# Kernel tuning notes

Hardware: AMD Instinct MI355X
Metric: run time of the kernel (lower is better)

Reference implementation:

```python
import math
import jax, jax.numpy as jnp
import numpy as np

B, S, D = 8, 920, 1536
H, HD = 4, 384            # num heads, head dim; all_head = H*HD = 1536
MAX_POS = 920
L = 2 * MAX_POS - 1       # 1839 relative positions


def setup_inputs() -> dict:
    key = jax.random.key(0)
    k1, k2, k3, k4, k5 = jax.random.split(key, 5)
    return {
        "hidden_states": jax.random.normal(k1, (B, S, D), dtype=jnp.float32),
        "w_query": jax.random.normal(k2, (D, H * HD), dtype=jnp.float32) * 0.02,
        "w_key": jax.random.normal(k3, (D, H * HD), dtype=jnp.float32) * 0.02,
        "w_value": jax.random.normal(k4, (D, H * HD), dtype=jnp.float32) * 0.02,
        "distance_embedding": jax.random.normal(k5, (L, HD), dtype=jnp.float32) * 0.02,
    }


def reshape_fortran(x, shape):
    # Matches torch reference: reverse-permute, C reshape of reversed shape, reverse-permute back.
    x = jnp.transpose(x, tuple(reversed(range(x.ndim))))
    x = jnp.reshape(x, tuple(reversed(shape)))
    return jnp.transpose(x, tuple(reversed(range(len(shape)))))


def relative_position_embedding_rotate(scores):
    # scores: [B, H, L, S]
    scores = jnp.transpose(scores, (0, 2, 3, 1))  # [B, L, S, H]
    b, hs, s, h = scores.shape
    scores = jnp.concatenate([scores, jnp.zeros((b, s, s, h), scores.dtype)], axis=1)
    scores = reshape_fortran(scores, [b, (hs + s) * s, 1, h])
    scores = scores[:, : (s + hs - 1) * s]
    scores = reshape_fortran(scores, [b, hs + s - 1, s, h])
    halfpoint = hs // 2
    scores = scores[:, halfpoint : halfpoint + s]          # [B, S, S, H]
    scores = jnp.transpose(scores, (0, 2, 1, 3))           # transpose(1,2)
    return jnp.transpose(scores, (0, 3, 1, 2))             # [B, H, S, S]


def reference(hidden_states, w_query, w_key, w_value, distance_embedding):
    inv = 1.0 / math.sqrt(HD)
    q = (hidden_states @ w_query) * inv                    # [B, S, H*HD]
    k = hidden_states @ w_key
    v = hidden_states @ w_value

    def heads(x):  # [B,S,H*HD] -> [B,H,S,HD]
        return jnp.transpose(x.reshape(B, S, H, HD), (0, 2, 1, 3))

    q, k, v = heads(q), heads(k), heads(v)

    scores = jnp.einsum("bhqd,bhkd->bhqk", q, k)           # [B,H,S,S]
    rel = jnp.einsum("ld,bhsd->bhls", distance_embedding, q)  # [B,H,L,S]
    scores = scores + relative_position_embedding_rotate(rel)

    probs = jax.nn.softmax(scores, axis=-1)
    ctx = jnp.einsum("bhqk,bhkd->bhqd", probs, v)          # [B,H,S,HD]
    ctx = jnp.transpose(ctx, (0, 2, 1, 3)).reshape(B, S, H * HD)
    return ctx
```

## Files before the change

kernel.cpp:

```cpp
#include <hip/hip_runtime.h>

#define S_LEN 920
#define DMODEL 1536
#define NH 4
#define HD 384
#define LREL 1839
#define BATCH 8
#define MTOT (BATCH * S_LEN)
#define KPAD 960
#define PRLD 1840
#define NBH (BATCH * NH)

#define CHS   5652480UL
#define BSLAB 2826240UL
#define KOFF  1413120UL

#define TP_BH   1692800UL
#define SCPR_BH 3385600UL
#define CHBH    (TP_BH + SCPR_BH)
#define QKV_SCRATCH 36765696UL
#define EB_BYTES 1412352UL
#define VT_BYTES 23592960UL

typedef __attribute__((ext_vector_type(8))) short  s16x8;
typedef __attribute__((ext_vector_type(4))) short  s16x4;
typedef __attribute__((ext_vector_type(8))) __bf16 bf16x8;
typedef __attribute__((ext_vector_type(4))) float  f32x4;

__device__ __forceinline__ short f2b(float x) {
  unsigned u = __builtin_bit_cast(unsigned, x);
  unsigned r = (u + 0x7FFFu + ((u >> 16) & 1u)) >> 16;
  return (short)r;
}
__device__ __forceinline__ float b2f(short s) {
  unsigned u = ((unsigned)(unsigned short)s) << 16;
  return __builtin_bit_cast(float, u);
}

__device__ __forceinline__ void load_lds16(const short* g, short* lds) {
  __builtin_amdgcn_global_load_lds(
      (const __attribute__((address_space(1))) void*)g,
      (__attribute__((address_space(3))) void*)lds, 16, 0, 0);
}

__device__ __forceinline__ f32x4 mfma_bf16(s16x8 a, s16x8 b, f32x4 c) {
  return __builtin_amdgcn_mfma_f32_16x16x32_bf16(
      __builtin_bit_cast(bf16x8, a), __builtin_bit_cast(bf16x8, b), c, 0, 0, 0);
}

__device__ __forceinline__ void gemm_core(short* As, short* Bs,
                                          const short* __restrict__ A, int ldA, int mClamp,
                                          const short* __restrict__ B, int ldB, int nClamp,
                                          int K, int m0, int n0, f32x4 acc[4][4]) {
  const int tid  = threadIdx.x;
  const int w    = tid >> 6;
  const int lane = tid & 63;
  const int lrow = lane >> 3;
  const int lcol = (lane & 7) * 8;
  const int lr   = lane & 15;
  const int lq   = lane >> 4;
  const int wm   = (w >> 1) * 64;
  const int wn   = (w & 1) * 64;

  const short* pa[4];
  const short* pb[4];
  short* la[4];
  short* lb[4];
#pragma unroll
  for (int i = 0; i < 4; ++i) {
    int row = w * 32 + i * 8 + lrow;
    int ra = m0 + row; if (ra > mClamp) ra = mClamp;
    int rb = n0 + row; if (rb > nClamp) rb = nClamp;
    pa[i] = A + (size_t)ra * ldA + lcol;
    pb[i] = B + (size_t)rb * ldB + lcol;
    la[i] = &As[(w * 32 + i * 8) * 64];
    lb[i] = &Bs[(w * 32 + i * 8) * 64];
  }

#pragma unroll
  for (int i = 0; i < 4; ++i)
#pragma unroll
    for (int j = 0; j < 4; ++j) acc[i][j] = (f32x4){0.f, 0.f, 0.f, 0.f};

  for (int k0 = 0; k0 < K; k0 += 64) {
#pragma unroll
    for (int i = 0; i < 4; ++i) {
      load_lds16(pa[i] + k0, la[i]);
      load_lds16(pb[i] + k0, lb[i]);
    }
    __syncthreads();
#pragma unroll
    for (int kk = 0; kk < 2; ++kk) {
      s16x8 af[4], bf[4];
#pragma unroll
      for (int f = 0; f < 4; ++f)
        af[f] = *(const s16x8*)&As[(wm + f * 16 + lr) * 64 + kk * 32 + lq * 8];
#pragma unroll
      for (int f = 0; f < 4; ++f)
        bf[f] = *(const s16x8*)&Bs[(wn + f * 16 + lr) * 64 + kk * 32 + lq * 8];
#pragma unroll
      for (int i = 0; i < 4; ++i)
#pragma unroll
        for (int j = 0; j < 4; ++j)
          acc[i][j] = mfma_bf16(af[i], bf[j], acc[i][j]);
    }
    __syncthreads();
  }
}

__device__ __forceinline__ void gemm_core256(short* As, short* Bs,
                                             const short* __restrict__ A, int ldA, int mClamp,
                                             const short* __restrict__ B, int ldB, int nClamp,
                                             int K, int m0, int n0, f32x4 acc[4][8]) {
  const int tid  = threadIdx.x;
  const int w    = tid >> 6;
  const int lane = tid & 63;
  const int lrow = lane >> 3;
  const int lcol = (lane & 7) * 8;
  const int lr   = lane & 15;
  const int lq   = lane >> 4;
  const int wm   = (w >> 1) * 64;
  const int wn   = (w & 1) * 128;

  const short* pa[4];
  short* la[4];
  const short* pb[8];
  short* lb[8];
#pragma unroll
  for (int i = 0; i < 4; ++i) {
    int row = w * 32 + i * 8 + lrow;
    int ra = m0 + row; if (ra > mClamp) ra = mClamp;
    pa[i] = A + (size_t)ra * ldA + lcol;
    la[i] = &As[(w * 32 + i * 8) * 64];
  }
#pragma unroll
  for (int i = 0; i < 8; ++i) {
    int row = w * 64 + i * 8 + lrow;
    int rb = n0 + row; if (rb > nClamp) rb = nClamp;
    pb[i] = B + (size_t)rb * ldB + lcol;
    lb[i] = &Bs[(w * 64 + i * 8) * 64];
  }

#pragma unroll
  for (int i = 0; i < 4; ++i)
#pragma unroll
    for (int j = 0; j < 8; ++j) acc[i][j] = (f32x4){0.f, 0.f, 0.f, 0.f};

  for (int k0 = 0; k0 < K; k0 += 64) {
#pragma unroll
    for (int i = 0; i < 4; ++i) load_lds16(pa[i] + k0, la[i]);
#pragma unroll
    for (int i = 0; i < 8; ++i) load_lds16(pb[i] + k0, lb[i]);
    __syncthreads();
#pragma unroll
    for (int kk = 0; kk < 2; ++kk) {
      s16x8 af[4], bf[8];
#pragma unroll
      for (int f = 0; f < 4; ++f)
        af[f] = *(const s16x8*)&As[(wm + f * 16 + lr) * 64 + kk * 32 + lq * 8];
#pragma unroll
      for (int f = 0; f < 8; ++f)
        bf[f] = *(const s16x8*)&Bs[(wn + f * 16 + lr) * 64 + kk * 32 + lq * 8];
#pragma unroll
      for (int i = 0; i < 4; ++i)
#pragma unroll
        for (int j = 0; j < 8; ++j)
          acc[i][j] = mfma_bf16(af[i], bf[j], acc[i][j]);
    }
    __syncthreads();
  }
}

__global__ void k_cast(const float* __restrict__ X, short* __restrict__ O, int n4) {
  int i = blockIdx.x * blockDim.x + threadIdx.x;
  if (i >= n4) return;
  float4 v = ((const float4*)X)[i];
  s16x4 o = {f2b(v.x), f2b(v.y), f2b(v.z), f2b(v.w)};
  *(s16x4*)&O[(size_t)i * 4] = o;
}

__global__ void k_transpose_w(const float* __restrict__ W0, const float* __restrict__ W1,
                              const float* __restrict__ W2, short* __restrict__ Wt) {
  const float* W = (blockIdx.z == 0) ? W0 : ((blockIdx.z == 1) ? W1 : W2);
  short* O = Wt + (size_t)blockIdx.z * DMODEL * DMODEL;
  __shared__ float t[32][33];
  int tx = threadIdx.x, ty = threadIdx.y;
  int n0 = blockIdx.x * 32, k0 = blockIdx.y * 32;
#pragma unroll
  for (int i = 0; i < 4; ++i)
    t[ty + i * 8][tx] = W[(size_t)(k0 + ty + i * 8) * DMODEL + n0 + tx];
  __syncthreads();
#pragma unroll
  for (int i = 0; i < 4; ++i)
    O[(size_t)(n0 + ty + i * 8) * DMODEL + k0 + tx] = f2b(t[tx][ty + i * 8]);
}

__global__ void k_zero_vtpad(short* __restrict__ Vt) {
  int idx = blockIdx.x * blockDim.x + threadIdx.x;
  if (idx >= NBH * HD * (KPAD - S_LEN)) return;
  int bhd = idx / (KPAD - S_LEN);
  int s = S_LEN + idx - bhd * (KPAD - S_LEN);
  Vt[(size_t)bhd * KPAD + s] = 0;
}

#define QKV_NT (DMODEL / 64)

__device__ __forceinline__ s16x8 qkv_frag(const short* base, int row, int kk, int lq) {
  int byte = (row << 7) + (kk << 6) + (lq << 4);
  byte ^= (row & 7) << 4;
  return *(const s16x8*)((const char*)base + byte);
}

__global__ __launch_bounds__(512, 2) void k_gemm_qkv(const short* __restrict__ Xb,
                                                     const short* __restrict__ Wt,
                                                     short* __restrict__ out16,
                                                     short* __restrict__ Vt) {
  __shared__ short smem[57344];
  short* const A0 = smem;
  short* const B0 = smem + 16384;
  short* const A1 = smem + 28672;
  short* const B1 = smem + 45056;

  const int z = blockIdx.z;
  const int t = blockIdx.x;
  const int t2 = (t & 7) * 29 + (t >> 3);
  const int m0 = (t2 >> 3) * 256;
  const int n0 = (t2 & 7) * 192;

  const int tid = threadIdx.x, w = tid >> 6, lane = tid & 63;
  const int lr = lane & 15, lq = lane >> 4;
  const int wr = w >> 1, wc = w & 1;

  const short* const Bg = Wt + (size_t)z * DMODEL * DMODEL;

  const short* pa[4]; int la[4];
  const short* pb[3]; int lb[3];
  {
    const int rl = lane >> 3, c = lane & 7;
#pragma unroll
    for (int i = 0; i < 4; ++i) {
      int r = w * 32 + i * 8 + rl;
      int ra = m0 + r; if (ra > MTOT - 1) ra = MTOT - 1;
      pa[i] = Xb + (size_t)ra * DMODEL + ((c ^ (r & 7)) * 8);
      la[i] = (w * 32 + i * 8) * 64;
    }
#pragma unroll
    for (int i = 0; i < 3; ++i) {
      int r = w * 24 + i * 8 + rl;
      pb[i] = Bg + (size_t)(n0 + r) * DMODEL + ((c ^ (r & 7)) * 8);
      lb[i] = (w * 24 + i * 8) * 64;
    }
  }

  f32x4 acc[4][6];
#pragma unroll
  for (int i = 0; i < 4; ++i)
#pragma unroll
    for (int j = 0; j < 6; ++j) acc[i][j] = (f32x4){0.f, 0.f, 0.f, 0.f};

#pragma unroll
  for (int i = 0; i < 4; ++i) load_lds16(pa[i], A0 + la[i]);
#pragma unroll
  for (int i = 0; i < 3; ++i) load_lds16(pb[i], B0 + lb[i]);

  for (int kt = 0; kt < QKV_NT; ++kt) {
    short* const Ab = (kt & 1) ? A1 : A0;
    short* const Bb = (kt & 1) ? B1 : B0;
    short* const An = (kt & 1) ? A0 : A1;
    short* const Bn = (kt & 1) ? B0 : B1;

    if (kt + 1 < QKV_NT) {
      const int k0 = (kt + 1) * 64;
#pragma unroll
      for (int i = 0; i < 4; ++i) load_lds16(pa[i] + k0, An + la[i]);
#pragma unroll
      for (int i = 0; i < 3; ++i) load_lds16(pb[i] + k0, Bn + lb[i]);
      asm volatile("s_waitcnt vmcnt(7)" ::: "memory");
    } else {
      asm volatile("s_waitcnt vmcnt(0)" ::: "memory");
    }
    __builtin_amdgcn_sched_barrier(0);
    __builtin_amdgcn_s_barrier();
    __builtin_amdgcn_sched_barrier(0);

    s16x8 a[4], bb[3];
#pragma unroll
    for (int f = 0; f < 4; ++f) a[f] = qkv_frag(Ab, wr * 64 + f * 16 + lr, 0, lq);
#pragma unroll
    for (int f = 0; f < 3; ++f) bb[f] = qkv_frag(Bb, wc * 96 + f * 16 + lr, 0, lq);
    __builtin_amdgcn_s_barrier();
    __builtin_amdgcn_s_setprio(1);
#pragma unroll
    for (int i = 0; i < 4; ++i)
#pragma unroll
      for (int j = 0; j < 3; ++j) acc[i][j] = mfma_bf16(a[i], bb[j], acc[i][j]);
    __builtin_amdgcn_s_setprio(0);
    __builtin_amdgcn_s_barrier();
#pragma unroll
    for (int f = 0; f < 3; ++f) bb[f] = qkv_frag(Bb, wc * 96 + (3 + f) * 16 + lr, 0, lq);
    __builtin_amdgcn_s_barrier();
    __builtin_amdgcn_s_setprio(1);
#pragma unroll
    for (int i = 0; i < 4; ++i)
#pragma unroll
      for (int j = 0; j < 3; ++j) acc[i][3 + j] = mfma_bf16(a[i], bb[j], acc[i][3 + j]);
    __builtin_amdgcn_s_setprio(0);
    __builtin_amdgcn_s_barrier();
#pragma unroll
    for (int f = 0; f < 4; ++f) a[f] = qkv_frag(Ab, wr * 64 + f * 16 + lr, 1, lq);
#pragma unroll
    for (int f = 0; f < 3; ++f) bb[f] = qkv_frag(Bb, wc * 96 + f * 16 + lr, 1, lq);
    __builtin_amdgcn_s_barrier();
    __builtin_amdgcn_s_setprio(1);
#pragma unroll
    for (int i = 0; i < 4; ++i)
#pragma unroll
      for (int j = 0; j < 3; ++j) acc[i][j] = mfma_bf16(a[i], bb[j], acc[i][j]);
    __builtin_amdgcn_s_setprio(0);
    __builtin_amdgcn_s_barrier();
#pragma unroll
    for (int f = 0; f < 3; ++f) bb[f] = qkv_frag(Bb, wc * 96 + (3 + f) * 16 + lr, 1, lq);
    __builtin_amdgcn_s_barrier();
    __builtin_amdgcn_s_setprio(1);
#pragma unroll
    for (int i = 0; i < 4; ++i)
#pragma unroll
      for (int j = 0; j < 3; ++j) acc[i][3 + j] = mfma_bf16(a[i], bb[j], acc[i][3 + j]);
    __builtin_amdgcn_s_setprio(0);
    __builtin_amdgcn_s_barrier();
  }

  __syncthreads();
  const float inv = 0.05103103630798287f;
  if (z != 2) {
    short* T = smem;
#pragma unroll
    for (int i = 0; i < 4; ++i)
#pragma unroll
      for (int j = 0; j < 6; ++j) {
        int ml = wr * 64 + i * 16 + lq * 4;
        int nl = wc * 96 + j * 16 + lr;
#pragma unroll
        for (int r = 0; r < 4; ++r) {
          float v = acc[i][j][r];
          T[(ml + r) * 200 + nl] = f2b(z == 0 ? v * inv : v);
        }
      }
    __syncthreads();
    for (int u = 0; u < 12; ++u) {
      int unit = u * 512 + tid;
      int ml = unit / 24, c = unit - ml * 24;
      int m = m0 + ml;
      if (m < MTOT) {
        int b = m / S_LEN, s = m - b * S_LEN;
        short* dst = out16 + (size_t)(b >> 1) * CHS + (size_t)(b & 1) * BSLAB +
                     (z == 1 ? KOFF : 0UL) + (size_t)s * DMODEL + n0 + c * 8;
        *(s16x8*)dst = *(const s16x8*)&T[ml * 200 + c * 8];
      }
    }
  } else {
    short* T = smem;
#pragma unroll
    for (int i = 0; i < 4; ++i)
#pragma unroll
      for (int j = 0; j < 6; ++j) {
        int ml = wr * 64 + i * 16 + lq * 4;
        int nl = wc * 96 + j * 16 + lr;
#pragma unroll
        for (int r = 0; r < 4; ++r)
          T[nl * 264 + ml + r] = f2b(acc[i][j][r]);
      }
    __syncthreads();
    const int h = n0 / HD;
    const int d0 = n0 - h * HD;
    for (int u = 0; u < 12; ++u) {
      int unit = u * 512 + tid;
      int nl = unit >> 5, c = unit & 31;
      int m = m0 + c * 8;
      if (m < MTOT) {
        int b = m / S_LEN, s = m - b * S_LEN;
        size_t row = (size_t)(b * NH + h) * HD + d0 + nl;
        *(s16x8*)&Vt[row * KPAD + s] = *(const s16x8*)&T[nl * 264 + c * 8];
      }
    }
  }
}

__global__ __launch_bounds__(256) void k_gemm_T(const short* __restrict__ out16,
                                                const short* __restrict__ Eb,
                                                short* __restrict__ Tp, int bh0) {
  __shared__ short smem[16384];
  const int z = blockIdx.z;
  const int bh = bh0 + z, b = bh >> 2, h = bh & 3;
  int t = blockIdx.x;
  int i_idx, j_idx;
  if (t < 7) { i_idx = t; j_idx = 6 - t; }
  else { int u = t - 7; int s = 7 + (u >> 3); i_idx = u & 7; j_idx = s - i_idx; }
  const int m0 = i_idx * 128, n0 = j_idx * 128;
  const short* A = out16 + (size_t)(b >> 1) * CHS + (size_t)(b & 1) * BSLAB + h * HD;
  f32x4 acc[4][4];
  gemm_core(smem, smem + 8192, A, DMODEL, S_LEN - 1, Eb, HD, LREL - 1, HD, m0, n0, acc);
  const int tid = threadIdx.x, w = tid >> 6, lane = tid & 63;
  const int lr = lane & 15, lq = lane >> 4;
  const int wm = (w >> 1) * 64, wn = (w & 1) * 64;
#pragma unroll
  for (int i = 0; i < 4; ++i)
#pragma unroll
    for (int j = 0; j < 4; ++j) {
      int l = n0 + wn + j * 16 + lr;
#pragma unroll
      for (int r = 0; r < 4; ++r) {
        int m = m0 + wm + i * 16 + lq * 4 + r;
        if (m < S_LEN) {
          int jp = l - (S_LEN - 1) + m;
          if (jp >= 0 && jp < S_LEN)
            Tp[((size_t)z * S_LEN + m) * S_LEN + jp] = f2b(acc[i][j][r]);
        }
      }
    }
}

__global__ __launch_bounds__(256, 2) void k_gemm_scores(const short* __restrict__ out16,
                                                        const short* __restrict__ Tp,
                                                        float* __restrict__ SCc, int bh0) {
  __shared__ short smem[24576];
  const int z = blockIdx.z;
  const int bh = bh0 + z, b = bh >> 2, h = bh & 3;
  const int m0 = blockIdx.x * 128, n0 = blockIdx.y * 256;
  const short* Qp = out16 + (size_t)(b >> 1) * CHS + (size_t)(b & 1) * BSLAB + h * HD;
  const short* Kp = Qp + KOFF;
  f32x4 acc[4][8];
  gemm_core256(smem, smem + 8192, Qp, DMODEL, S_LEN - 1, Kp, DMODEL, S_LEN - 1,
               HD, m0, n0, acc);
  const int tid = threadIdx.x, w = tid >> 6, lane = tid & 63;
  const int lr = lane & 15, lq = lane >> 4;
  const int wm = (w >> 1) * 64, wn = (w & 1) * 128;
#pragma unroll
  for (int i = 0; i < 4; ++i)
#pragma unroll
    for (int j = 0; j < 8; ++j) {
      int n = n0 + wn + j * 16 + lr;
#pragma unroll
      for (int r = 0; r < 4; ++r) {
        int m = m0 + wm + i * 16 + lq * 4 + r;
        if (m < S_LEN && n < S_LEN) {
          SCc[((size_t)z * S_LEN + m) * S_LEN + n] =
              acc[i][j][r] + b2f(Tp[((size_t)z * S_LEN + m) * S_LEN + n]);
        }
      }
    }
}

__global__ __launch_bounds__(256) void k_softmax(float* __restrict__ SCc) {
  const int row = blockIdx.x;
  float* src = SCc + (size_t)row * S_LEN;
  short* dst = (short*)src;
  const int tid = threadIdx.x, lane = tid & 63, wv = tid >> 6;
  float v[4];
#pragma unroll
  for (int i = 0; i < 4; ++i) {
    int k = i * 256 + tid;
    v[i] = (k < S_LEN) ? src[k] : -1e30f;
  }
  float mx = fmaxf(fmaxf(v[0], v[1]), fmaxf(v[2], v[3]));
  for (int off = 32; off; off >>= 1) mx = fmaxf(mx, __shfl_xor(mx, off));
  __shared__ float redm[4];
  __shared__ float reds[4];
  if (lane == 0) redm[wv] = mx;
  __syncthreads();
  mx = fmaxf(fmaxf(redm[0], redm[1]), fmaxf(redm[2], redm[3]));
  float e[4], s = 0.f;
#pragma unroll
  for (int i = 0; i < 4; ++i) { e[i] = __expf(v[i] - mx); s += e[i]; }
  for (int off = 32; off; off >>= 1) s += __shfl_xor(s, off);
  if (lane == 0) reds[wv] = s;
  __syncthreads();
  s = reds[0] + reds[1] + reds[2] + reds[3];
  float rs = 1.0f / s;
#pragma unroll
  for (int i = 0; i < 4; ++i) {
    int k = i * 256 + tid;
    if (k < KPAD) dst[k] = f2b(k < S_LEN ? e[i] * rs : 0.f);
  }
}

__global__ __launch_bounds__(256) void k_gemm_ctx(const short* __restrict__ PRc,
                                                  const short* __restrict__ Vt,
                                                  float* __restrict__ out, int bh0) {
  __shared__ short smem[16384];
  const int z = blockIdx.z;
  const int bh = bh0 + z, b = bh >> 2, h = bh & 3;
  const int m0 = blockIdx.x * 128, n0 = blockIdx.y * 128;
  const short* A = PRc + (size_t)z * S_LEN * PRLD;
  const short* Bt = Vt + (size_t)bh * HD * KPAD;
  f32x4 acc[4][4];
  gemm_core(smem, smem + 8192, A, PRLD, S_LEN - 1, Bt, KPAD, HD - 1, KPAD, m0, n0, acc);
  const int tid = threadIdx.x, w = tid >> 6, lane = tid & 63;
  const int lr = lane & 15, lq = lane >> 4;
  const int wm = (w >> 1) * 64, wn = (w & 1) * 64;
#pragma unroll
  for (int i = 0; i < 4; ++i)
#pragma unroll
    for (int j = 0; j < 4; ++j) {
      int n = n0 + wn + j * 16 + lr;
#pragma unroll
      for (int r = 0; r < 4; ++r) {
        int m = m0 + wm + i * 16 + lq * 4 + r;
        if (m < S_LEN)
          out[((size_t)(b * S_LEN) + m) * DMODEL + h * HD + n] = acc[i][j][r];
      }
    }
}

extern "C" void kernel_launch(void* const* d_in, const int* in_sizes, int n_in,
                              void* d_out, int out_size, void* d_ws, size_t ws_size,
                              hipStream_t stream) {
  const float* hs = (const float*)d_in[0];
  const float* wq = (const float*)d_in[1];
  const float* wk = (const float*)d_in[2];
  const float* wv = (const float*)d_in[3];
  const float* de = (const float*)d_in[4];
  char* ws = (char*)d_ws;

  int CH;
  if      (ws_size >= 32 * CHBH + EB_BYTES + VT_BYTES) CH = 32;
  else if (ws_size >= 16 * CHBH + EB_BYTES + VT_BYTES) CH = 16;
  else                                                  CH = 8;
  size_t chunk_bytes = (size_t)CH * CHBH;
  size_t fixed_base = chunk_bytes > QKV_SCRATCH ? chunk_bytes : QKV_SCRATCH;

  short* Xb  = (short*)(ws + 0);
  short* Wt  = (short*)(ws + 22609920UL);
  short* Tp  = (short*)(ws + 0);
  float* SCc = (float*)(ws + (size_t)CH * TP_BH);
  short* PRc = (short*)SCc;
  short* Eb  = (short*)(ws + fixed_base);
  short* Vt  = (short*)(ws + fixed_base + EB_BYTES);
  short* out16 = (short*)d_out;

  k_cast<<<(MTOT * DMODEL / 4 + 255) / 256, 256, 0, stream>>>(hs, Xb, MTOT * DMODEL / 4);
  k_cast<<<(LREL * HD / 4 + 255) / 256, 256, 0, stream>>>(de, Eb, LREL * HD / 4);
  k_transpose_w<<<dim3(48, 48, 3), dim3(32, 8, 1), 0, stream>>>(wq, wk, wv, Wt);
  k_zero_vtpad<<<(NBH * HD * (KPAD - S_LEN) + 255) / 256, 256, 0, stream>>>(Vt);

  k_gemm_qkv<<<dim3(232, 1, 3), 512, 0, stream>>>(Xb, Wt, out16, Vt);

  int NC = 32 / CH;
  for (int c = 0; c < NC; ++c) {
    int bh0 = c * CH;
    k_gemm_T<<<dim3(71, 1, CH), 256, 0, stream>>>(out16, Eb, Tp, bh0);
    k_gemm_scores<<<dim3(8, 4, CH), 256, 0, stream>>>(out16, Tp, SCc, bh0);
    k_softmax<<<CH * S_LEN, 256, 0, stream>>>(SCc);
    k_gemm_ctx<<<dim3(8, 3, CH), 256, 0, stream>>>(PRc, Vt, (float*)d_out, bh0);
  }
}
```

Before: 504.4 us.

## Reuse double-buffered swizzled 256x192 GEMM pipeline for T, scores and ctx kernels

Moves the QKV projection's double-buffered, XOR-swizzled, setprio-interleaved MFMA main loop into a templated gemm_pipe and uses it for the relative-position T GEMM, the QK scores GEMM and the PV context GEMM, replacing their single-buffered 128x128 or 128x256 cores. Tiles become 256x192 with 512 threads, so prefetch of the next K slice overlaps compute and LDS bank conflicts are reduced. The T GEMM grid is re-enumerated to cover only the diagonal band of tiles that feed the rotated output. Softmax now reads float4 and writes four bf16 values per thread. Larger tiles mean fewer blocks and more padding waste at the 920 boundary, which may hurt occupancy on the smaller GEMMs.

```diff
diff --git a/kernel.cpp b/kernel.cpp
--- a/kernel.cpp
+++ b/kernel.cpp
@@ -48,126 +48,121 @@
       __builtin_bit_cast(bf16x8, a), __builtin_bit_cast(bf16x8, b), c, 0, 0, 0);
 }
 
-__device__ __forceinline__ void gemm_core(short* As, short* Bs,
-                                          const short* __restrict__ A, int ldA, int mClamp,
-                                          const short* __restrict__ B, int ldB, int nClamp,
-                                          int K, int m0, int n0, f32x4 acc[4][4]) {
-  const int tid  = threadIdx.x;
-  const int w    = tid >> 6;
-  const int lane = tid & 63;
-  const int lrow = lane >> 3;
-  const int lcol = (lane & 7) * 8;
-  const int lr   = lane & 15;
-  const int lq   = lane >> 4;
-  const int wm   = (w >> 1) * 64;
-  const int wn   = (w & 1) * 64;
-
-  const short* pa[4];
-  const short* pb[4];
-  short* la[4];
-  short* lb[4];
-#pragma unroll
-  for (int i = 0; i < 4; ++i) {
-    int row = w * 32 + i * 8 + lrow;
-    int ra = m0 + row; if (ra > mClamp) ra = mClamp;
-    int rb = n0 + row; if (rb > nClamp) rb = nClamp;
-    pa[i] = A + (size_t)ra * ldA + lcol;
-    pb[i] = B + (size_t)rb * ldB + lcol;
-    la[i] = &As[(w * 32 + i * 8) * 64];
-    lb[i] = &Bs[(w * 32 + i * 8) * 64];
-  }
-
-#pragma unroll
-  for (int i = 0; i < 4; ++i)
-#pragma unroll
-    for (int j = 0; j < 4; ++j) acc[i][j] = (f32x4){0.f, 0.f, 0.f, 0.f};
-
-  for (int k0 = 0; k0 < K; k0 += 64) {
+__device__ __forceinline__ s16x8 frag_swz(const short* base, int row, int kk, int lq) {
+  int byte = (row << 7) + (kk << 6) + (lq << 4);
+  byte ^= (row & 7) << 4;
+  return *(const s16x8*)((const char*)base + byte);
+}
+
+template <int NT>
+__device__ __forceinline__ void gemm_pipe(short* smem,
+    const short* __restrict__ A, int ldA, int mClamp, int m0,
+    const short* __restrict__ B, int ldB, int nClamp, int n0,
+    f32x4 acc[4][6]) {
+  short* const A0 = smem;
+  short* const B0 = smem + 16384;
+  short* const A1 = smem + 28672;
+  short* const B1 = smem + 45056;
+
+  const int tid = threadIdx.x, w = tid >> 6, lane = tid & 63;
+  const int lr = lane & 15, lq = lane >> 4;
+  const int wr = w >> 1, wc = w & 1;
+
+  const short* pa[4]; int la[4];
+  const short* pb[3]; int lb[3];
+  {
+    const int rl = lane >> 3, c = lane & 7;
 #pragma unroll
     for (int i = 0; i < 4; ++i) {
-      load_lds16(pa[i] + k0, la[i]);
-      load_lds16(pb[i] + k0, lb[i]);
-    }
-    __syncthreads();
-#pragma unroll
-    for (int kk = 0; kk < 2; ++kk) {
-      s16x8 af[4], bf[4];
-#pragma unroll
-      for (int f = 0; f < 4; ++f)
-        af[f] = *(const s16x8*)&As[(wm + f * 16 + lr) * 64 + kk * 32 + lq * 8];
-#pragma unroll
-      for (int f = 0; f < 4; ++f)
-        bf[f] = *(const s16x8*)&Bs[(wn + f * 16 + lr) * 64 + kk * 32 + lq * 8];
-#pragma unroll
-      for (int i = 0; i < 4; ++i)
-#pragma unroll
-        for (int j = 0; j < 4; ++j)
-          acc[i][j] = mfma_bf16(af[i], bf[j], acc[i][j]);
-    }
-    __syncthreads();
-  }
-}
-
-__device__ __forceinline__ void gemm_core256(short* As, short* Bs,
-                                             const short* __restrict__ A, int ldA, int mClamp,
-                                             const short* __restrict__ B, int ldB, int nClamp,
-                                             int K, int m0, int n0, f32x4 acc[4][8]) {
-  const int tid  = threadIdx.x;
-  const int w    = tid >> 6;
-  const int lane = tid & 63;
-  const int lrow = lane >> 3;
-  const int lcol = (lane & 7) * 8;
-  const int lr   = lane & 15;
-  const int lq   = lane >> 4;
-  const int wm   = (w >> 1) * 64;
-  const int wn   = (w & 1) * 128;
-
-  const short* pa[4];
-  short* la[4];
-  const short* pb[8];
-  short* lb[8];
-#pragma unroll
-  for (int i = 0; i < 4; ++i) {
-    int row = w * 32 + i * 8 + lrow;
-    int ra = m0 + row; if (ra > mClamp) ra = mClamp;
-    pa[i] = A + (size_t)ra * ldA + lcol;
-    la[i] = &As[(w * 32 + i * 8) * 64];
-  }
-#pragma unroll
-  for (int i = 0; i < 8; ++i) {
-    int row = w * 64 + i * 8 + lrow;
-    int rb = n0 + row; if (rb > nClamp) rb = nClamp;
-    pb[i] = B + (size_t)rb * ldB + lcol;
-    lb[i] = &Bs[(w * 64 + i * 8) * 64];
-  }
-
-#pragma unroll
-  for (int i = 0; i < 4; ++i)
-#pragma unroll
-    for (int j = 0; j < 8; ++j) acc[i][j] = (f32x4){0.f, 0.f, 0.f, 0.f};
-
-  for (int k0 = 0; k0 < K; k0 += 64) {
-#pragma unroll
-    for (int i = 0; i < 4; ++i) load_lds16(pa[i] + k0, la[i]);
-#pragma unroll
-    for (int i = 0; i < 8; ++i) load_lds16(pb[i] + k0, lb[i]);
-    __syncthreads();
-#pragma unroll
-    for (int kk = 0; kk < 2; ++kk) {
-      s16x8 af[4], bf[8];
-#pragma unroll
-      for (int f = 0; f < 4; ++f)
-        af[f] = *(const s16x8*)&As[(wm + f * 16 + lr) * 64 + kk * 32 + lq * 8];
-#pragma unroll
-      for (int f = 0; f < 8; ++f)
-        bf[f] = *(const s16x8*)&Bs[(wn + f * 16 + lr) * 64 + kk * 32 + lq * 8];
-#pragma unroll
-      for (int i = 0; i < 4; ++i)
-#pragma unroll
-        for (int j = 0; j < 8; ++j)
-          acc[i][j] = mfma_bf16(af[i], bf[j], acc[i][j]);
-    }
-    __syncthreads();
+      int r = w * 32 + i * 8 + rl;
+      int ra = m0 + r; if (ra > mClamp) ra = mClamp;
+      pa[i] = A + (size_t)ra * ldA + ((c ^ (r & 7)) * 8);
+      la[i] = (w * 32 + i * 8) * 64;
+    }
+#pragma unroll
+    for (int i = 0; i < 3; ++i) {
+      int r = w * 24 + i * 8 + rl;
+      int rb = n0 + r; if (rb > nClamp) rb = nClamp;
+      pb[i] = B + (size_t)rb * ldB + ((c ^ (r & 7)) * 8);
+      lb[i] = (w * 24 + i * 8) * 64;
+    }
+  }
+
+#pragma unroll
+  for (int i = 0; i < 4; ++i)
+#pragma unroll
+    for (int j = 0; j < 6; ++j) acc[i][j] = (f32x4){0.f, 0.f, 0.f, 0.f};
+
+#pragma unroll
+  for (int i = 0; i < 4; ++i) load_lds16(pa[i], A0 + la[i]);
+#pragma unroll
+  for (int i = 0; i < 3; ++i) load_lds16(pb[i], B0 + lb[i]);
+
+  for (int kt = 0; kt < NT; ++kt) {
+    short* const Ab = (kt & 1) ? A1 : A0;
+    short* const Bb = (kt & 1) ? B1 : B0;
+    short* const An = (kt & 1) ? A0 : A1;
+    short* const Bn = (kt & 1) ? B0 : B1;
+
+    if (kt + 1 < NT) {
+      const int k0 = (kt + 1) * 64;
+#pragma unroll
+      for (int i = 0; i < 4; ++i) load_lds16(pa[i] + k0, An + la[i]);
+#pragma unroll
+      for (int i = 0; i < 3; ++i) load_lds16(pb[i] + k0, Bn + lb[i]);
+      asm volatile("s_waitcnt vmcnt(7)" ::: "memory");
+    } else {
+      asm volatile("s_waitcnt vmcnt(0)" ::: "memory");
+    }
+    __builtin_amdgcn_sched_barrier(0);
+    __builtin_amdgcn_s_barrier();
+    __builtin_amdgcn_sched_barrier(0);
+
+    s16x8 a[4], bb[3];
+#pragma unroll
+    for (int f = 0; f < 4; ++f) a[f] = frag_swz(Ab, wr * 64 + f * 16 + lr, 0, lq);
+#pragma unroll
+    for (int f = 0; f < 3; ++f) bb[f] = frag_swz(Bb, wc * 96 + f * 16 + lr, 0, lq);
+    __builtin_amdgcn_s_barrier();
+    __builtin_amdgcn_s_setprio(1);
+#pragma unroll
+    for (int i = 0; i < 4; ++i)
+#pragma unroll
+      for (int j = 0; j < 3; ++j) acc[i][j] = mfma_bf16(a[i], bb[j], acc[i][j]);
+    __builtin_amdgcn_s_setprio(0);
+    __builtin_amdgcn_s_barrier();
+#pragma unroll
+    for (int f = 0; f < 3; ++f) bb[f] = frag_swz(Bb, wc * 96 + (3 + f) * 16 + lr, 0, lq);
+    __builtin_amdgcn_s_barrier();
+    __builtin_amdgcn_s_setprio(1);
+#pragma unroll
+    for (int i = 0; i < 4; ++i)
+#pragma unroll
+      for (int j = 0; j < 3; ++j) acc[i][3 + j] = mfma_bf16(a[i], bb[j], acc[i][3 + j]);
+    __builtin_amdgcn_s_setprio(0);
+    __builtin_amdgcn_s_barrier();
+#pragma unroll
+    for (int f = 0; f < 4; ++f) a[f] = frag_swz(Ab, wr * 64 + f * 16 + lr, 1, lq);
+#pragma unroll
+    for (int f = 0; f < 3; ++f) bb[f] = frag_swz(Bb, wc * 96 + f * 16 + lr, 1, lq);
+    __builtin_amdgcn_s_barrier();
+    __builtin_amdgcn_s_setprio(1);
+#pragma unroll
+    for (int i = 0; i < 4; ++i)
+#pragma unroll
+      for (int j = 0; j < 3; ++j) acc[i][j] = mfma_bf16(a[i], bb[j], acc[i][j]);
+    __builtin_amdgcn_s_setprio(0);
+    __builtin_amdgcn_s_barrier();
+#pragma unroll
+    for (int f = 0; f < 3; ++f) bb[f] = frag_swz(Bb, wc * 96 + (3 + f) * 16 + lr, 1, lq);
+    __builtin_amdgcn_s_barrier();
+    __builtin_amdgcn_s_setprio(1);
+#pragma unroll
+    for (int i = 0; i < 4; ++i)
+#pragma unroll
+      for (int j = 0; j < 3; ++j) acc[i][3 + j] = mfma_bf16(a[i], bb[j], acc[i][3 + j]);
+    __builtin_amdgcn_s_setprio(0);
+    __builtin_amdgcn_s_barrier();
   }
 }
 
@@ -205,22 +200,11 @@
 
 #define QKV_NT (DMODEL / 64)
 
-__device__ __forceinline__ s16x8 qkv_frag(const short* base, int row, int kk, int lq) {
-  int byte = (row << 7) + (kk << 6) + (lq << 4);
-  byte ^= (row & 7) << 4;
-  return *(const s16x8*)((const char*)base + byte);
-}
-
 __global__ __launch_bounds__(512, 2) void k_gemm_qkv(const short* __restrict__ Xb,
                                                      const short* __restrict__ Wt,
                                                      short* __restrict__ out16,
                                                      short* __restrict__ Vt) {
   __shared__ short smem[57344];
-  short* const A0 = smem;
-  short* const B0 = smem + 16384;
-  short* const A1 = smem + 28672;
-  short* const B1 = smem + 45056;
-
   const int z = blockIdx.z;
   const int t = blockIdx.x;
   const int t2 = (t & 7) * 29 + (t >> 3);
@@ -231,104 +215,9 @@
   const int lr = lane & 15, lq = lane >> 4;
   const int wr = w >> 1, wc = w & 1;
 
-  const short* const Bg = Wt + (size_t)z * DMODEL * DMODEL;
-
-  const short* pa[4]; int la[4];
-  const short* pb[3]; int lb[3];
-  {
-    const int rl = lane >> 3, c = lane & 7;
-#pragma unroll
-    for (int i = 0; i < 4; ++i) {
-      int r = w * 32 + i * 8 + rl;
-      int ra = m0 + r; if (ra > MTOT - 1) ra = MTOT - 1;
-      pa[i] = Xb + (size_t)ra * DMODEL + ((c ^ (r & 7)) * 8);
-      la[i] = (w * 32 + i * 8) * 64;
-    }
-#pragma unroll
-    for (int i = 0; i < 3; ++i) {
-      int r = w * 24 + i * 8 + rl;
-      pb[i] = Bg + (size_t)(n0 + r) * DMODEL + ((c ^ (r & 7)) * 8);
-      lb[i] = (w * 24 + i * 8) * 64;
-    }
-  }
-
   f32x4 acc[4][6];
-#pragma unroll
-  for (int i = 0; i < 4; ++i)
-#pragma unroll
-    for (int j = 0; j < 6; ++j) acc[i][j] = (f32x4){0.f, 0.f, 0.f, 0.f};
-
-#pragma unroll
-  for (int i = 0; i < 4; ++i) load_lds16(pa[i], A0 + la[i]);
-#pragma unroll
-  for (int i = 0; i < 3; ++i) load_lds16(pb[i], B0 + lb[i]);
-
-  for (int kt = 0; kt < QKV_NT; ++kt) {
-    short* const Ab = (kt & 1) ? A1 : A0;
-    short* const Bb = (kt & 1) ? B1 : B0;
-    short* const An = (kt & 1) ? A0 : A1;
-    short* const Bn = (kt & 1) ? B0 : B1;
-
-    if (kt + 1 < QKV_NT) {
-      const int k0 = (kt + 1) * 64;
-#pragma unroll
-      for (int i = 0; i < 4; ++i) load_lds16(pa[i] + k0, An + la[i]);
-#pragma unroll
-      for (int i = 0; i < 3; ++i) load_lds16(pb[i] + k0, Bn + lb[i]);
-      asm volatile("s_waitcnt vmcnt(7)" ::: "memory");
-    } else {
-      asm volatile("s_waitcnt vmcnt(0)" ::: "memory");
-    }
-    __builtin_amdgcn_sched_barrier(0);
-    __builtin_amdgcn_s_barrier();
-    __builtin_amdgcn_sched_barrier(0);
-
-    s16x8 a[4], bb[3];
-#pragma unroll
-    for (int f = 0; f < 4; ++f) a[f] = qkv_frag(Ab, wr * 64 + f * 16 + lr, 0, lq);
-#pragma unroll
-    for (int f = 0; f < 3; ++f) bb[f] = qkv_frag(Bb, wc * 96 + f * 16 + lr, 0, lq);
-    __builtin_amdgcn_s_barrier();
-    __builtin_amdgcn_s_setprio(1);
-#pragma unroll
-    for (int i = 0; i < 4; ++i)
-#pragma unroll
-      for (int j = 0; j < 3; ++j) acc[i][j] = mfma_bf16(a[i], bb[j], acc[i][j]);
-    __builtin_amdgcn_s_setprio(0);
-    __builtin_amdgcn_s_barrier();
-#pragma unroll
-    for (int f = 0; f < 3; ++f) bb[f] = qkv_frag(Bb, wc * 96 + (3 + f) * 16 + lr, 0, lq);
-    __builtin_amdgcn_s_barrier();
-    __builtin_amdgcn_s_setprio(1);
-#pragma unroll
-    for (int i = 0; i < 4; ++i)
-#pragma unroll
-      for (int j = 0; j < 3; ++j) acc[i][3 + j] = mfma_bf16(a[i], bb[j], acc[i][3 + j]);
-    __builtin_amdgcn_s_setprio(0);
-    __builtin_amdgcn_s_barrier();
-#pragma unroll
-    for (int f = 0; f < 4; ++f) a[f] = qkv_frag(Ab, wr * 64 + f * 16 + lr, 1, lq);
-#pragma unroll
-    for (int f = 0; f < 3; ++f) bb[f] = qkv_frag(Bb, wc * 96 + f * 16 + lr, 1, lq);
-    __builtin_amdgcn_s_barrier();
-    __builtin_amdgcn_s_setprio(1);
-#pragma unroll
-    for (int i = 0; i < 4; ++i)
-#pragma unroll
-      for (int j = 0; j < 3; ++j) acc[i][j] = mfma_bf16(a[i], bb[j], acc[i][j]);
-    __builtin_amdgcn_s_setprio(0);
-    __builtin_amdgcn_s_barrier();
-#pragma unroll
-    for (int f = 0; f < 3; ++f) bb[f] = qkv_frag(Bb, wc * 96 + (3 + f) * 16 + lr, 1, lq);
-    __builtin_amdgcn_s_barrier();
-    __builtin_amdgcn_s_setprio(1);
-#pragma unroll
-    for (int i = 0; i < 4; ++i)
-#pragma unroll
-      for (int j = 0; j < 3; ++j) acc[i][3 + j] = mfma_bf16(a[i], bb[j], acc[i][3 + j]);
-    __builtin_amdgcn_s_setprio(0);
-    __builtin_amdgcn_s_barrier();
-  }
+  gemm_pipe<QKV_NT>(smem, Xb, DMODEL, MTOT - 1, m0,
+                    Wt + (size_t)z * DMODEL * DMODEL, DMODEL, DMODEL - 1, n0, acc);
 
   __syncthreads();
   const float inv = 0.05103103630798287f;
@@ -386,31 +275,35 @@
   }
 }
 
-__global__ __launch_bounds__(256) void k_gemm_T(const short* __restrict__ out16,
-                                                const short* __restrict__ Eb,
-                                                short* __restrict__ Tp, int bh0) {
-  __shared__ short smem[16384];
+__global__ __launch_bounds__(512, 2) void k_gemm_T(const short* __restrict__ out16,
+                                                   const short* __restrict__ Eb,
+                                                   short* __restrict__ Tp, int bh0) {
+  __shared__ short smem[57344];
   const int z = blockIdx.z;
   const int bh = bh0 + z, b = bh >> 2, h = bh & 3;
-  int t = blockIdx.x;
-  int i_idx, j_idx;
-  if (t < 7) { i_idx = t; j_idx = 6 - t; }
-  else { int u = t - 7; int s = 7 + (u >> 3); i_idx = u & 7; j_idx = s - i_idx; }
-  const int m0 = i_idx * 128, n0 = j_idx * 128;
+  const int t = blockIdx.x;
+  int mi, lj;
+  if      (t < 7)  { mi = 0; lj = 3 + t; }
+  else if (t < 14) { mi = 1; lj = 2 + (t - 7); }
+  else if (t < 21) { mi = 2; lj = t - 14; }
+  else             { mi = 3; lj = t - 21; }
+  const int m0 = mi * 256, n0 = lj * 192;
   const short* A = out16 + (size_t)(b >> 1) * CHS + (size_t)(b & 1) * BSLAB + h * HD;
-  f32x4 acc[4][4];
-  gemm_core(smem, smem + 8192, A, DMODEL, S_LEN - 1, Eb, HD, LREL - 1, HD, m0, n0, acc);
+
+  f32x4 acc[4][6];
+  gemm_pipe<HD / 64>(smem, A, DMODEL, S_LEN - 1, m0, Eb, HD, LREL - 1, n0, acc);
+
   const int tid = threadIdx.x, w = tid >> 6, lane = tid & 63;
   const int lr = lane & 15, lq = lane >> 4;
-  const int wm = (w >> 1) * 64, wn = (w & 1) * 64;
-#pragma unroll
-  for (int i = 0; i < 4; ++i)
-#pragma unroll
-    for (int j = 0; j < 4; ++j) {
-      int l = n0 + wn + j * 16 + lr;
+  const int wr = w >> 1, wc = w & 1;
+#pragma unroll
+  for (int i = 0; i < 4; ++i)
+#pragma unroll
+    for (int j = 0; j < 6; ++j) {
+      int l = n0 + wc * 96 + j * 16 + lr;
 #pragma unroll
       for (int r = 0; r < 4; ++r) {
-        int m = m0 + wm + i * 16 + lq * 4 + r;
+        int m = m0 + wr * 64 + i * 16 + lq * 4 + r;
         if (m < S_LEN) {
           int jp = l - (S_LEN - 1) + m;
           if (jp >= 0 && jp < S_LEN)
@@ -420,29 +313,30 @@
     }
 }
 
-__global__ __launch_bounds__(256, 2) void k_gemm_scores(const short* __restrict__ out16,
+__global__ __launch_bounds__(512, 2) void k_gemm_scores(const short* __restrict__ out16,
                                                         const short* __restrict__ Tp,
                                                         float* __restrict__ SCc, int bh0) {
-  __shared__ short smem[24576];
+  __shared__ short smem[57344];
   const int z = blockIdx.z;
   const int bh = bh0 + z, b = bh >> 2, h = bh & 3;
-  const int m0 = blockIdx.x * 128, n0 = blockIdx.y * 256;
+  const int m0 = blockIdx.x * 256, n0 = blockIdx.y * 192;
   const short* Qp = out16 + (size_t)(b >> 1) * CHS + (size_t)(b & 1) * BSLAB + h * HD;
   const short* Kp = Qp + KOFF;
-  f32x4 acc[4][8];
-  gemm_core256(smem, smem + 8192, Qp, DMODEL, S_LEN - 1, Kp, DMODEL, S_LEN - 1,
-               HD, m0, n0, acc);
+
+  f32x4 acc[4][6];
+  gemm_pipe<HD / 64>(smem, Qp, DMODEL, S_LEN - 1, m0, Kp, DMODEL, S_LEN - 1, n0, acc);
+
   const int tid = threadIdx.x, w = tid >> 6, lane = tid & 63;
   const int lr = lane & 15, lq = lane >> 4;
-  const int wm = (w >> 1) * 64, wn = (w & 1) * 128;
-#pragma unroll
-  for (int i = 0; i < 4; ++i)
-#pragma unroll
-    for (int j = 0; j < 8; ++j) {
-      int n = n0 + wn + j * 16 + lr;
+  const int wr = w >> 1, wc = w & 1;
+#pragma unroll
+  for (int i = 0; i < 4; ++i)
+#pragma unroll
+    for (int j = 0; j < 6; ++j) {
+      int n = n0 + wc * 96 + j * 16 + lr;
 #pragma unroll
       for (int r = 0; r < 4; ++r) {
-        int m = m0 + wm + i * 16 + lq * 4 + r;
+        int m = m0 + wr * 64 + i * 16 + lq * 4 + r;
         if (m < S_LEN && n < S_LEN) {
           SCc[((size_t)z * S_LEN + m) * S_LEN + n] =
               acc[i][j][r] + b2f(Tp[((size_t)z * S_LEN + m) * S_LEN + n]);
@@ -456,11 +350,13 @@
   float* src = SCc + (size_t)row * S_LEN;
   short* dst = (short*)src;
   const int tid = threadIdx.x, lane = tid & 63, wv = tid >> 6;
+  const bool act = tid < 230;
   float v[4];
-#pragma unroll
-  for (int i = 0; i < 4; ++i) {
-    int k = i * 256 + tid;
-    v[i] = (k < S_LEN) ? src[k] : -1e30f;
+  if (act) {
+    float4 f = ((const float4*)src)[tid];
+    v[0] = f.x; v[1] = f.y; v[2] = f.z; v[3] = f.w;
+  } else {
+    v[0] = v[1] = v[2] = v[3] = -1e30f;
   }
   float mx = fmaxf(fmaxf(v[0], v[1]), fmaxf(v[2], v[3]));
   for (int off = 32; off; off >>= 1) mx = fmaxf(mx, __shfl_xor(mx, off));
@@ -477,35 +373,41 @@
   __syncthreads();
   s = reds[0] + reds[1] + reds[2] + reds[3];
   float rs = 1.0f / s;
-#pragma unroll
-  for (int i = 0; i < 4; ++i) {
-    int k = i * 256 + tid;
-    if (k < KPAD) dst[k] = f2b(k < S_LEN ? e[i] * rs : 0.f);
-  }
-}
-
-__global__ __launch_bounds__(256) void k_gemm_ctx(const short* __restrict__ PRc,
-                                                  const short* __restrict__ Vt,
-                                                  float* __restrict__ out, int bh0) {
-  __shared__ short smem[16384];
+  if (tid < 240) {
+    s16x4 o;
+    if (act) {
+      o = (s16x4){f2b(e[0] * rs), f2b(e[1] * rs), f2b(e[2] * rs), f2b(e[3] * rs)};
+    } else {
+      o = (s16x4){0, 0, 0, 0};
+    }
+    *(s16x4*)&dst[tid * 4] = o;
+  }
+}
+
+__global__ __launch_bounds__(512, 2) void k_gemm_ctx(const short* __restrict__ PRc,
+                                                     const short* __restrict__ Vt,
+                                                     float* __restrict__ out, int bh0) {
+  __shared__ short smem[57344];
   const int z = blockIdx.z;
   const int bh = bh0 + z, b = bh >> 2, h = bh & 3;
-  const int m0 = blockIdx.x * 128, n0 = blockIdx.y * 128;
+  const int m0 = blockIdx.x * 256, n0 = blockIdx.y * 192;
   const short* A = PRc + (size_t)z * S_LEN * PRLD;
   const short* Bt = Vt + (size_t)bh * HD * KPAD;
-  f32x4 acc[4][4];
-  gemm_core(smem, smem + 8192, A, PRLD, S_LEN - 1, Bt, KPAD, HD - 1, KPAD, m0, n0, acc);
+
+  f32x4 acc[4][6];
+  gemm_pipe<KPAD / 64>(smem, A, PRLD, S_LEN - 1, m0, Bt, KPAD, HD - 1, n0, acc);
+
   const int tid = threadIdx.x, w = tid >> 6, lane = tid & 63;
   const int lr = lane & 15, lq = lane >> 4;
-  const int wm = (w >> 1) * 64, wn = (w & 1) * 64;
-#pragma unroll
-  for (int i = 0; i < 4; ++i)
-#pragma unroll
-    for (int j = 0; j < 4; ++j) {
-      int n = n0 + wn + j * 16 + lr;
+  const int wr = w >> 1, wc = w & 1;
+#pragma unroll
+  for (int i = 0; i < 4; ++i)
+#pragma unroll
+    for (int j = 0; j < 6; ++j) {
+      int n = n0 + wc * 96 + j * 16 + lr;
 #pragma unroll
       for (int r = 0; r < 4; ++r) {
-        int m = m0 + wm + i * 16 + lq * 4 + r;
+        int m = m0 + wr * 64 + i * 16 + lq * 4 + r;
         if (m < S_LEN)
           out[((size_t)(b * S_LEN) + m) * DMODEL + h * HD + n] = acc[i][j][r];
       }
@@ -548,9 +450,9 @@
   int NC = 32 / CH;
   for (int c = 0; c < NC; ++c) {
     int bh0 = c * CH;
-    k_gemm_T<<<dim3(71, 1, CH), 256, 0, stream>>>(out16, Eb, Tp, bh0);
-    k_gemm_scores<<<dim3(8, 4, CH), 256, 0, stream>>>(out16, Tp, SCc, bh0);
+    k_gemm_T<<<dim3(27, 1, CH), 512, 0, stream>>>(out16, Eb, Tp, bh0);
+    k_gemm_scores<<<dim3(4, 5, CH), 512, 0, stream>>>(out16, Tp, SCc, bh0);
     k_softmax<<<CH * S_LEN, 256, 0, stream>>>(SCc);
-    k_gemm_ctx<<<dim3(8, 3, CH), 256, 0, stream>>>(PRc, Vt, (float*)d_out, bh0);
-  }
-}
+    k_gemm_ctx<<<dim3(4, 2, CH), 512, 0, stream>>>(PRc, Vt, (float*)d_out, bh0);
+  }
+}
```

After: 505.6 us. Within noise of the previous version (+0.2%).
